# Performance work log

Measured on AMD Instinct MI355X. Metric: run time of the kernel, lower is better.

The kernel has to match this reference:

```python
import jax, jax.numpy as jnp
import numpy as np
import math

NUM_HEADS = 16
SEGMENT_SIZE = 128
DILATION = 2


def hilbert_map(seq_len: int) -> np.ndarray:
    """Boustrophedon ('Hilbert') permutation, matching the torch reference."""
    if seq_len <= 64:
        return np.arange(seq_len, dtype=np.int64)
    g = int(math.ceil(math.sqrt(seq_len)))
    fm = np.zeros(seq_len, dtype=np.int64)
    idx = 0
    for row in range(g):
        cols = range(g) if row % 2 == 0 else range(g - 1, -1, -1)
        for col in cols:
            lp = row * g + col
            if lp < seq_len and idx < seq_len:
                fm[lp] = idx
                idx += 1
    return fm


def setup_inputs() -> dict:
    key = jax.random.key(0)
    k1, k2, k3 = jax.random.split(key, 3)
    B, S, D = 2, 8192, 1024
    x = jax.random.normal(k1, (B, S, D), dtype=jnp.float32)
    W_qkv = jax.random.normal(k2, (D, 3 * D), dtype=jnp.float32) * 0.02
    W_out = jax.random.normal(k3, (D, D), dtype=jnp.float32) * 0.02
    return {"x": x, "W_qkv": W_qkv, "W_out": W_out}


def reference(x, W_qkv, W_out):
    B, S, Dm = x.shape
    H, Dh = NUM_HEADS, Dm // NUM_HEADS
    seg, dil = SEGMENT_SIZE, DILATION
    scale = Dh ** -0.5

    qkv = (x @ W_qkv).reshape(B, S, 3, H, Dh)
    q = jnp.transpose(qkv[:, :, 0], (0, 2, 1, 3))  # [B,H,S,Dh]
    k = jnp.transpose(qkv[:, :, 1], (0, 2, 1, 3))
    v = jnp.transpose(qkv[:, :, 2], (0, 2, 1, 3))

    # Hilbert reorder (active since S > 64)
    m = jnp.asarray(hilbert_map(S))
    q, k, v = q[:, :, m], k[:, :, m], v[:, :, m]

    # Vectorized segment-local dilated attention (S % seg == 0 here)
    nseg = S // seg
    qs = q.reshape(B, H, nseg, seg, Dh)
    ks = k.reshape(B, H, nseg, seg, Dh)[:, :, :, ::dil]  # dilated keys
    vs = v.reshape(B, H, nseg, seg, Dh)[:, :, :, ::dil]
    scores = jnp.einsum('bhnqd,bhnkd->bhnqk', qs, ks) * scale
    attn = jax.nn.softmax(scores, axis=-1)
    out = jnp.einsum('bhnqk,bhnkd->bhnqd', attn, vs).reshape(B, H, S, Dh)

    # Reverse Hilbert ordering
    inv = jnp.argsort(m)
    out = out[:, :, inv]

    out = jnp.transpose(out, (0, 2, 1, 3)).reshape(B, S, Dm)
    return out @ W_out
```

## Files before the change

kernel.cpp:

```cpp
#include <hip/hip_runtime.h>
#include <stdint.h>

typedef unsigned short ushort_t;
typedef __bf16 bf16x8 __attribute__((ext_vector_type(8)));
typedef float  f32x4  __attribute__((ext_vector_type(4)));
typedef float  f32x16 __attribute__((ext_vector_type(16)));

#define DEV static __device__ __forceinline__

DEV ushort_t f2bf(float f){
  union { float f; unsigned u; } x; x.f = f;
  unsigned u = x.u;
  return (ushort_t)((u + 0x7fffu + ((u >> 16) & 1u)) >> 16);
}

DEV int hmap(int p){
  int r = p / 91;
  int c = p - r * 91;
  return (r & 1) ? (r * 91 + 90 - c) : p;
}

DEV void async16(const void* g, void* l){
  __builtin_amdgcn_global_load_lds(
      (const __attribute__((address_space(1))) unsigned*)g,
      (__attribute__((address_space(3))) unsigned*)l, 16, 0, 0);
}

template<int GATHER>
DEV int arow_map(int r){
  if (GATHER == 0) return r;
  if (GATHER == 1){ int b = r >> 13, p = r & 8191; return b * 8192 + hmap(p); }
  int b = r >> 12, rem = r & 4095, seg = rem >> 6, j = rem & 63;
  return b * 8192 + hmap(seg * 128 + 2 * j);
}

__global__ void cast_kernel(const float* __restrict__ in, ushort_t* __restrict__ out, int n4){
  int i = blockIdx.x * blockDim.x + threadIdx.x;
  if (i < n4){
    float4 v = ((const float4*)in)[i];
    ushort4 o;
    o.x = f2bf(v.x); o.y = f2bf(v.y); o.z = f2bf(v.z); o.w = f2bf(v.w);
    ((ushort4*)out)[i] = o;
  }
}

__global__ void transpose_cast(const float* __restrict__ W, ushort_t* __restrict__ WT,
                               int rows, int cols){
  __shared__ ushort_t t[64 * 66];
  int tid = threadIdx.x;
  int c0 = blockIdx.x * 64, r0 = blockIdx.y * 64;
  int cl = tid & 63, rb = tid >> 6;
  for (int i = 0; i < 16; ++i){
    int r = rb + i * 4;
    t[r * 66 + cl] = f2bf(W[(size_t)(r0 + r) * cols + c0 + cl]);
  }
  __syncthreads();
  int rr = tid & 63, cb = tid >> 6;
  for (int i = 0; i < 16; ++i){
    int cc = cb + i * 4;
    WT[(size_t)(c0 + cc) * rows + r0 + rr] = t[rr * 66 + cc];
  }
}

template<int OUT_BF16, int GATHER>
__global__ __launch_bounds__(256) void gemm_bt(const ushort_t* __restrict__ A,
                                               const ushort_t* __restrict__ BT,
                                               void* __restrict__ Cout,
                                               int M, int N, int K){
  __shared__ ushort_t As[128 * 64];
  __shared__ ushort_t Bs[128 * 64];
  int tid  = threadIdx.x;
  int lane = tid & 63, w = tid >> 6;
  int l31 = lane & 31, lh = lane >> 5;

  int nx = gridDim.x, gy = gridDim.y;
  int flat = blockIdx.y * nx + blockIdx.x;
  int xcd = flat & 7, lid = flat >> 3;
  int chunk = nx * 4;
  int sub = lid / chunk, rem = lid - sub * chunk;
  int mt = xcd * (gy >> 3) + sub * 4 + (rem & 3);
  int nt = rem >> 2;
  int m0 = mt * 128, n0 = nt * 128;

  int wm = (w >> 1) * 64, wn = (w & 1) * 64;

  f32x16 acc[2][2];
  for (int a = 0; a < 4; ++a) for (int b = 0; b < 16; ++b) acc[a >> 1][a & 1][b] = 0.f;

  int rbase = tid >> 3, slot = tid & 7;
  size_t asrc[4], bsrc[4];
  #pragma unroll
  for (int i = 0; i < 4; ++i){
    int r = rbase + 32 * i;
    int g = slot ^ (r & 7);
    asrc[i] = (size_t)arow_map<GATHER>(m0 + r) * K + g * 8;
    bsrc[i] = (size_t)(n0 + r) * K + g * 8;
  }

  int aoff[2][4], boff[2][4];
  #pragma unroll
  for (int mi = 0; mi < 2; ++mi){
    int r = wm + mi * 32 + l31;
    for (int kc = 0; kc < 4; ++kc)
      aoff[mi][kc] = r * 64 + ((kc * 2 + lh) ^ (r & 7)) * 8;
  }
  #pragma unroll
  for (int ni = 0; ni < 2; ++ni){
    int r = wn + ni * 32 + l31;
    for (int kc = 0; kc < 4; ++kc)
      boff[ni][kc] = r * 64 + ((kc * 2 + lh) ^ (r & 7)) * 8;
  }

  for (int k0 = 0; k0 < K; k0 += 64){
    __syncthreads();
    #pragma unroll
    for (int i = 0; i < 4; ++i)
      async16(&A[asrc[i] + k0], &As[(size_t)(256 * i + tid) * 8]);
    #pragma unroll
    for (int i = 0; i < 4; ++i)
      async16(&BT[bsrc[i] + k0], &Bs[(size_t)(256 * i + tid) * 8]);
    __syncthreads();

    #pragma unroll
    for (int kc = 0; kc < 4; ++kc){
      bf16x8 af[2], bg[2];
      af[0] = *(const bf16x8*)&As[aoff[0][kc]];
      af[1] = *(const bf16x8*)&As[aoff[1][kc]];
      bg[0] = *(const bf16x8*)&Bs[boff[0][kc]];
      bg[1] = *(const bf16x8*)&Bs[boff[1][kc]];
      #pragma unroll
      for (int mi = 0; mi < 2; ++mi)
        #pragma unroll
        for (int ni = 0; ni < 2; ++ni)
          acc[mi][ni] = __builtin_amdgcn_mfma_f32_32x32x16_bf16(af[mi], bg[ni], acc[mi][ni], 0, 0, 0);
    }
  }

  #pragma unroll
  for (int mi = 0; mi < 2; ++mi){
    #pragma unroll
    for (int ni = 0; ni < 2; ++ni){
      f32x16 v = acc[mi][ni];
      #pragma unroll
      for (int reg = 0; reg < 16; ++reg){
        int r = m0 + wm + mi * 32 + (reg & 3) + 8 * (reg >> 2) + 4 * lh;
        size_t idx = (size_t)r * N + n0 + wn + ni * 32 + l31;
        if (OUT_BF16) ((ushort_t*)Cout)[idx] = f2bf(v[reg]);
        else          ((float*)   Cout)[idx] = v[reg];
      }
    }
  }
}

__global__ __launch_bounds__(256) void attn_kernel(const ushort_t* __restrict__ Qb,
                                                   const ushort_t* __restrict__ KV,
                                                   ushort_t* __restrict__ aout){
  __shared__ ushort_t Qs[128 * 72];
  __shared__ ushort_t Ks[64 * 72];
  __shared__ ushort_t Vt[64 * 72];
  int tid  = threadIdx.x;
  int lane = tid & 63, w = tid >> 6;
  int qd = lane >> 4, md = lane & 15;
  int seg = blockIdx.x, h = blockIdx.y, b = blockIdx.z;
  int p0 = seg * 128;

  for (int it = 0; it < 4; ++it){
    int q = it * 256 + tid;
    int r = q >> 3, ch = q & 7;
    uint4 d = *(const uint4*)&Qb[(size_t)(b * 8192 + p0 + r) * 1024 + h * 64 + ch * 8];
    *(uint4*)&Qs[r * 72 + ch * 8] = d;
  }
  for (int it = 0; it < 2; ++it){
    int q = it * 256 + tid;
    int r = q >> 3, ch = q & 7;
    uint4 d = *(const uint4*)&KV[(size_t)(b * 4096 + seg * 64 + r) * 2048 + h * 64 + ch * 8];
    *(uint4*)&Ks[r * 72 + ch * 8] = d;
  }
  for (int it = 0; it < 2; ++it){
    int q = it * 256 + tid;
    int r = q >> 3, ch = q & 7;
    union { uint4 v; ushort_t u[8]; } d;
    d.v = *(const uint4*)&KV[(size_t)(b * 4096 + seg * 64 + r) * 2048 + 1024 + h * 64 + ch * 8];
    for (int e = 0; e < 8; ++e) Vt[(ch * 8 + e) * 72 + r] = d.u[e];
  }
  __syncthreads();

  f32x4 z = {0.f, 0.f, 0.f, 0.f};
  f32x4 sc[2][4];
  for (int mi = 0; mi < 2; ++mi) for (int ni = 0; ni < 4; ++ni) sc[mi][ni] = z;
  for (int kc = 0; kc < 2; ++kc){
    bf16x8 aq[2], bk[4];
    for (int mi = 0; mi < 2; ++mi)
      aq[mi] = *(const bf16x8*)&Qs[(w * 32 + mi * 16 + md) * 72 + kc * 32 + qd * 8];
    for (int ni = 0; ni < 4; ++ni)
      bk[ni] = *(const bf16x8*)&Ks[(ni * 16 + md) * 72 + kc * 32 + qd * 8];
    for (int mi = 0; mi < 2; ++mi)
      for (int ni = 0; ni < 4; ++ni)
        sc[mi][ni] = __builtin_amdgcn_mfma_f32_16x16x32_bf16(aq[mi], bk[ni], sc[mi][ni], 0, 0, 0);
  }

  const float scale = 0.125f;
  ushort_t* Ps = Qs;
  for (int mi = 0; mi < 2; ++mi){
    for (int i = 0; i < 4; ++i){
      float mx = sc[mi][0][i];
      for (int ni = 1; ni < 4; ++ni) mx = fmaxf(mx, sc[mi][ni][i]);
      for (int d = 1; d < 16; d <<= 1) mx = fmaxf(mx, __shfl_xor(mx, d));
      float e[4], sum = 0.f;
      for (int ni = 0; ni < 4; ++ni){ e[ni] = __expf((sc[mi][ni][i] - mx) * scale); sum += e[ni]; }
      for (int d = 1; d < 16; d <<= 1) sum += __shfl_xor(sum, d);
      float inv = 1.0f / sum;
      int r = w * 32 + mi * 16 + qd * 4 + i;
      for (int ni = 0; ni < 4; ++ni)
        Ps[r * 72 + ni * 16 + md] = f2bf(e[ni] * inv);
    }
  }

  f32x4 oc[2][4];
  for (int mi = 0; mi < 2; ++mi) for (int ni = 0; ni < 4; ++ni) oc[mi][ni] = z;
  for (int kc = 0; kc < 2; ++kc){
    bf16x8 ap[2], bv[4];
    for (int mi = 0; mi < 2; ++mi)
      ap[mi] = *(const bf16x8*)&Ps[(w * 32 + mi * 16 + md) * 72 + kc * 32 + qd * 8];
    for (int ni = 0; ni < 4; ++ni)
      bv[ni] = *(const bf16x8*)&Vt[(ni * 16 + md) * 72 + kc * 32 + qd * 8];
    for (int mi = 0; mi < 2; ++mi)
      for (int ni = 0; ni < 4; ++ni)
        oc[mi][ni] = __builtin_amdgcn_mfma_f32_16x16x32_bf16(ap[mi], bv[ni], oc[mi][ni], 0, 0, 0);
  }

  for (int mi = 0; mi < 2; ++mi){
    for (int i = 0; i < 4; ++i){
      int rl = w * 32 + mi * 16 + qd * 4 + i;
      for (int ni = 0; ni < 4; ++ni)
        Ps[rl * 72 + ni * 16 + md] = f2bf(oc[mi][ni][i]);
    }
  }
  __syncthreads();
  for (int it = 0; it < 4; ++it){
    int q = it * 256 + tid;
    int r = q >> 3, ch = q & 7;
    int s = hmap(p0 + r);
    *(uint4*)&aout[(size_t)(b * 8192 + s) * 1024 + h * 64 + ch * 8] =
        *(const uint4*)&Qs[r * 72 + ch * 8];
  }
}

extern "C" void kernel_launch(void* const* d_in, const int* in_sizes, int n_in,
                              void* d_out, int out_size, void* d_ws, size_t ws_size,
                              hipStream_t stream){
  const float* x    = (const float*)d_in[0];
  const float* Wqkv = (const float*)d_in[1];
  const float* Wout = (const float*)d_in[2];
  float* out = (float*)d_out;

  char* ws = (char*)d_ws;
  ushort_t* xb    = (ushort_t*)(ws);
  ushort_t* WqT   = (ushort_t*)(ws + 33554432);
  ushort_t* WoT   = (ushort_t*)(ws + 39845888);
  ushort_t* Qbuf  = (ushort_t*)(ws + 41943040);
  ushort_t* KVbuf = (ushort_t*)(ws + 75497472);
  ushort_t* aoutb = (ushort_t*)(ws + 109051904);

  cast_kernel<<<16384, 256, 0, stream>>>(x, xb, (16384 * 1024) / 4);
  transpose_cast<<<dim3(48, 16), 256, 0, stream>>>(Wqkv, WqT, 1024, 3072);
  transpose_cast<<<dim3(16, 16), 256, 0, stream>>>(Wout, WoT, 1024, 1024);
  gemm_bt<1, 1><<<dim3(8, 128), 256, 0, stream>>>(xb, WqT, Qbuf, 16384, 1024, 1024);
  gemm_bt<1, 2><<<dim3(16, 64), 256, 0, stream>>>(xb, WqT + (size_t)1024 * 1024, KVbuf, 8192, 2048, 1024);
  attn_kernel<<<dim3(64, 16, 2), 256, 0, stream>>>(Qbuf, KVbuf, aoutb);
  gemm_bt<0, 0><<<dim3(8, 128), 256, 0, stream>>>(aoutb, WoT, out, 16384, 1024, 1024);
}
```

Measured before the change: 297.9 us.

## Widen GEMM tiles to 128x256 and switch to linear 1D block mapping

New measurement: 278.4 us. 6.5% less time.

```diff
diff --git a/kernel.cpp b/kernel.cpp
--- a/kernel.cpp
+++ b/kernel.cpp
@@ -63,50 +63,49 @@
 }
 
 template<int OUT_BF16, int GATHER>
-__global__ __launch_bounds__(256) void gemm_bt(const ushort_t* __restrict__ A,
-                                               const ushort_t* __restrict__ BT,
-                                               void* __restrict__ Cout,
-                                               int M, int N, int K){
+__global__ __launch_bounds__(256, 2) void gemm_bt(const ushort_t* __restrict__ A,
+                                                  const ushort_t* __restrict__ BT,
+                                                  void* __restrict__ Cout,
+                                                  int M, int N, int K){
   __shared__ ushort_t As[128 * 64];
-  __shared__ ushort_t Bs[128 * 64];
+  __shared__ ushort_t Bs[256 * 64];
   int tid  = threadIdx.x;
   int lane = tid & 63, w = tid >> 6;
   int l31 = lane & 31, lh = lane >> 5;
 
-  int nx = gridDim.x, gy = gridDim.y;
-  int flat = blockIdx.y * nx + blockIdx.x;
-  int xcd = flat & 7, lid = flat >> 3;
-  int chunk = nx * 4;
-  int sub = lid / chunk, rem = lid - sub * chunk;
-  int mt = xcd * (gy >> 3) + sub * 4 + (rem & 3);
-  int nt = rem >> 2;
-  int m0 = mt * 128, n0 = nt * 128;
-
-  int wm = (w >> 1) * 64, wn = (w & 1) * 64;
-
-  f32x16 acc[2][2];
-  for (int a = 0; a < 4; ++a) for (int b = 0; b < 16; ++b) acc[a >> 1][a & 1][b] = 0.f;
+  int mtc = M >> 7;
+  int o  = blockIdx.x;
+  int nt = o / mtc, mt = o - nt * mtc;
+  int m0 = mt * 128, n0 = nt * 256;
+
+  int wm = (w >> 1) * 64, wn = (w & 1) * 128;
+
+  f32x16 acc[2][4];
+  #pragma unroll
+  for (int a = 0; a < 8; ++a)
+    #pragma unroll
+    for (int b = 0; b < 16; ++b) acc[a >> 2][a & 3][b] = 0.f;
 
   int rbase = tid >> 3, slot = tid & 7;
-  size_t asrc[4], bsrc[4];
-  #pragma unroll
-  for (int i = 0; i < 4; ++i){
-    int r = rbase + 32 * i;
-    int g = slot ^ (r & 7);
-    asrc[i] = (size_t)arow_map<GATHER>(m0 + r) * K + g * 8;
-    bsrc[i] = (size_t)(n0 + r) * K + g * 8;
-  }
-
-  int aoff[2][4], boff[2][4];
+  int g0 = (slot ^ (rbase & 7)) * 8;
+  size_t asrc[4];
+  #pragma unroll
+  for (int i = 0; i < 4; ++i)
+    asrc[i] = (size_t)arow_map<GATHER>(m0 + rbase + 32 * i) * K + g0;
+  size_t bsrc0 = (size_t)(n0 + rbase) * K + g0;
+
+  int aoff[2][4], boff[4][4];
   #pragma unroll
   for (int mi = 0; mi < 2; ++mi){
     int r = wm + mi * 32 + l31;
+    #pragma unroll
     for (int kc = 0; kc < 4; ++kc)
       aoff[mi][kc] = r * 64 + ((kc * 2 + lh) ^ (r & 7)) * 8;
   }
   #pragma unroll
-  for (int ni = 0; ni < 2; ++ni){
+  for (int ni = 0; ni < 4; ++ni){
     int r = wn + ni * 32 + l31;
+    #pragma unroll
     for (int kc = 0; kc < 4; ++kc)
       boff[ni][kc] = r * 64 + ((kc * 2 + lh) ^ (r & 7)) * 8;
   }
@@ -117,21 +116,22 @@
     for (int i = 0; i < 4; ++i)
       async16(&A[asrc[i] + k0], &As[(size_t)(256 * i + tid) * 8]);
     #pragma unroll
-    for (int i = 0; i < 4; ++i)
-      async16(&BT[bsrc[i] + k0], &Bs[(size_t)(256 * i + tid) * 8]);
+    for (int i = 0; i < 8; ++i)
+      async16(&BT[bsrc0 + (size_t)(32 * i) * K + k0], &Bs[(size_t)(256 * i + tid) * 8]);
     __syncthreads();
 
     #pragma unroll
     for (int kc = 0; kc < 4; ++kc){
-      bf16x8 af[2], bg[2];
+      bf16x8 af[2], bg[4];
       af[0] = *(const bf16x8*)&As[aoff[0][kc]];
       af[1] = *(const bf16x8*)&As[aoff[1][kc]];
-      bg[0] = *(const bf16x8*)&Bs[boff[0][kc]];
-      bg[1] = *(const bf16x8*)&Bs[boff[1][kc]];
+      #pragma unroll
+      for (int ni = 0; ni < 4; ++ni)
+        bg[ni] = *(const bf16x8*)&Bs[boff[ni][kc]];
       #pragma unroll
       for (int mi = 0; mi < 2; ++mi)
         #pragma unroll
-        for (int ni = 0; ni < 2; ++ni)
+        for (int ni = 0; ni < 4; ++ni)
           acc[mi][ni] = __builtin_amdgcn_mfma_f32_32x32x16_bf16(af[mi], bg[ni], acc[mi][ni], 0, 0, 0);
     }
   }
@@ -139,7 +139,7 @@
   #pragma unroll
   for (int mi = 0; mi < 2; ++mi){
     #pragma unroll
-    for (int ni = 0; ni < 2; ++ni){
+    for (int ni = 0; ni < 4; ++ni){
       f32x16 v = acc[mi][ni];
       #pragma unroll
       for (int reg = 0; reg < 16; ++reg){
@@ -265,8 +265,8 @@
   cast_kernel<<<16384, 256, 0, stream>>>(x, xb, (16384 * 1024) / 4);
   transpose_cast<<<dim3(48, 16), 256, 0, stream>>>(Wqkv, WqT, 1024, 3072);
   transpose_cast<<<dim3(16, 16), 256, 0, stream>>>(Wout, WoT, 1024, 1024);
-  gemm_bt<1, 1><<<dim3(8, 128), 256, 0, stream>>>(xb, WqT, Qbuf, 16384, 1024, 1024);
-  gemm_bt<1, 2><<<dim3(16, 64), 256, 0, stream>>>(xb, WqT + (size_t)1024 * 1024, KVbuf, 8192, 2048, 1024);
+  gemm_bt<1, 1><<<4 * 128, 256, 0, stream>>>(xb, WqT, Qbuf, 16384, 1024, 1024);
+  gemm_bt<1, 2><<<8 * 64, 256, 0, stream>>>(xb, WqT + (size_t)1024 * 1024, KVbuf, 8192, 2048, 1024);
   attn_kernel<<<dim3(64, 16, 2), 256, 0, stream>>>(Qbuf, KVbuf, aoutb);
-  gemm_bt<0, 0><<<dim3(8, 128), 256, 0, stream>>>(aoutb, WoT, out, 16384, 1024, 1024);
-}
+  gemm_bt<0, 0><<<4 * 128, 256, 0, stream>>>(aoutb, WoT, out, 16384, 1024, 1024);
+}
```
